# Kernel tuning notes

Hardware: AMD Instinct MI355X
Metric: run time of the kernel (lower is better)

## Reference

```python
import jax, jax.numpy as jnp
import numpy as np

DIM = 2048
N_HEADS = 32
N_KV_HEADS = 8
HEAD_DIM = 64
N_REP = N_HEADS // N_KV_HEADS
SEQ = 2048
BATCH = 1


def _llama3_scaled_rope(head_dim, end, base=10000.0, scale_factor=8):
    # matches executorch precompute_freqs_cis with use_scaled=True
    freqs = 1.0 / (base ** (np.arange(0, head_dim, 2)[: head_dim // 2] / head_dim))
    low_freq_factor, high_freq_factor, old_ctx = 1.0, 4.0, 8192.0
    low_wl = old_ctx / low_freq_factor
    high_wl = old_ctx / high_freq_factor
    wavelen = 2.0 * np.pi / freqs
    smooth = (old_ctx / wavelen - low_freq_factor) / (high_freq_factor - low_freq_factor)
    scaled = np.where(
        wavelen < high_wl,
        freqs,
        np.where(wavelen > low_wl, freqs / scale_factor,
                 (1.0 - smooth) * freqs / scale_factor + smooth * freqs),
    )
    t = np.arange(end, dtype=np.float64)
    ang = np.outer(t, scaled)
    return np.cos(ang).astype(np.float32), np.sin(ang).astype(np.float32)


def setup_inputs() -> dict:
    key = jax.random.key(0)
    kx, kq, kk, kv, ko = jax.random.split(key, 5)
    x = jax.random.normal(kx, (BATCH, SEQ, DIM), dtype=jnp.float32)
    sc = 0.02
    wq = jax.random.normal(kq, (N_HEADS * HEAD_DIM, DIM), dtype=jnp.float32) * sc
    wk = jax.random.normal(kk, (N_KV_HEADS * HEAD_DIM, DIM), dtype=jnp.float32) * sc
    wv = jax.random.normal(kv, (N_KV_HEADS * HEAD_DIM, DIM), dtype=jnp.float32) * sc
    wo = jax.random.normal(ko, (N_HEADS * HEAD_DIM, DIM), dtype=jnp.float32).T * sc
    cos, sin = _llama3_scaled_rope(HEAD_DIM, SEQ)
    return {"x": x, "freqs_cos": jnp.asarray(cos), "freqs_sin": jnp.asarray(sin),
            "wq": wq, "wk": wk, "wv": wv, "wo": wo}


def _apply_rotary(x, cos, sin):
    # x: [b, s, h, hd]; cos/sin: [s, hd//2]; interleaved-pair RoPE
    xr = x[..., 0::2]
    xi = x[..., 1::2]
    c = cos[None, :, None, :]
    s = sin[None, :, None, :]
    out_r = xr * c - xi * s
    out_i = xr * s + xi * c
    return jnp.stack([out_r, out_i], axis=-1).reshape(x.shape)


def reference(x, freqs_cos, freqs_sin, wq, wk, wv, wo):
    b, s, _ = x.shape
    q = (x @ wq.T).reshape(b, s, N_HEADS, HEAD_DIM)
    k = (x @ wk.T).reshape(b, s, N_KV_HEADS, HEAD_DIM)
    v = (x @ wv.T).reshape(b, s, N_KV_HEADS, HEAD_DIM)
    q = _apply_rotary(q, freqs_cos, freqs_sin)
    k = _apply_rotary(k, freqs_cos, freqs_sin)
    # [b, h, s, hd]
    q = q.transpose(0, 2, 1, 3)
    k = k.transpose(0, 2, 1, 3)
    v = v.transpose(0, 2, 1, 3)
    # GQA: repeat_interleave over head dim
    k = jnp.repeat(k, N_REP, axis=1)
    v = jnp.repeat(v, N_REP, axis=1)
    scale = 1.0 / jnp.sqrt(jnp.asarray(HEAD_DIM, dtype=x.dtype))
    scores = jnp.einsum("bhqd,bhkd->bhqk", q, k) * scale
    causal = jnp.tril(jnp.ones((s, s), dtype=bool))
    scores = jnp.where(causal[None, None], scores, jnp.finfo(scores.dtype).min)
    attn = jax.nn.softmax(scores, axis=-1)
    y = jnp.einsum("bhqk,bhkd->bhqd", attn, v)
    y = y.transpose(0, 2, 1, 3).reshape(b, s, N_HEADS * HEAD_DIM)
    return y @ wo.T
```

## Files before the change

kernel.cpp:

```cpp
#include <hip/hip_runtime.h>
#include <hip/hip_bf16.h>

typedef __attribute__((ext_vector_type(8))) __bf16 bf16x8;
typedef __attribute__((ext_vector_type(4))) __bf16 bf16x4;
typedef __attribute__((ext_vector_type(4))) float f32x4;

#define DIM 2048
#define SEQ 2048
#define NH 32
#define NKV 8
#define HD 64
#define QKVD 3072
#define KOFF 2048
#define VOFF 2560
#define KVDIM 512

__device__ __forceinline__ void gld16(const __bf16* g, __bf16* l) {
    __builtin_amdgcn_global_load_lds(
        (const __attribute__((address_space(1))) void*)g,
        (__attribute__((address_space(3))) void*)l, 16, 0, 0);
}

__global__ void cvt_f32_bf16(const float* __restrict__ in, __bf16* __restrict__ out, int n4) {
    int i = blockIdx.x * blockDim.x + threadIdx.x;
    if (i < n4) {
        float4 v = reinterpret_cast<const float4*>(in)[i];
        bf16x4 o;
        o[0] = (__bf16)v.x; o[1] = (__bf16)v.y; o[2] = (__bf16)v.z; o[3] = (__bf16)v.w;
        reinterpret_cast<bf16x4*>(out)[i] = o;
    }
}

__global__ __launch_bounds__(256) void transpose_v(const __bf16* __restrict__ V,
                                                   __bf16* __restrict__ VT) {
    __shared__ __bf16 t[64][72];
    const int tid = threadIdx.x;
    const int r = tid >> 2, c0 = (tid & 3) * 16;
    const int sb = blockIdx.x * 64;
    const int db = blockIdx.y * 64;
    bf16x8 a0 = *reinterpret_cast<const bf16x8*>(V + (size_t)(sb + r) * QKVD + db + c0);
    bf16x8 a1 = *reinterpret_cast<const bf16x8*>(V + (size_t)(sb + r) * QKVD + db + c0 + 8);
#pragma unroll
    for (int e = 0; e < 8; ++e) { t[c0 + e][r] = a0[e]; t[c0 + 8 + e][r] = a1[e]; }
    __syncthreads();
    bf16x8 o0 = *reinterpret_cast<const bf16x8*>(&t[r][c0]);
    bf16x8 o1 = *reinterpret_cast<const bf16x8*>(&t[r][c0 + 8]);
    *reinterpret_cast<bf16x8*>(VT + (size_t)(db + r) * SEQ + sb + c0) = o0;
    *reinterpret_cast<bf16x8*>(VT + (size_t)(db + r) * SEQ + sb + c0 + 8) = o1;
}

template <typename OutT, bool ROPE>
__global__ __launch_bounds__(256) void gemm_tn(const __bf16* __restrict__ A,
                                               const __bf16* __restrict__ B,
                                               OutT* __restrict__ C,
                                               int M, int N, int K,
                                               float scale, int scaleNlim,
                                               const float* __restrict__ fc,
                                               const float* __restrict__ fs) {
    __shared__ __align__(16) __bf16 As[2][2][128 * 32];
    __shared__ __align__(16) __bf16 Bs[2][2][64 * 32];
    const int tid = threadIdx.x;
    const int lane = tid & 63;
    const int w = tid >> 6;
    const int l15 = lane & 15, lhi = lane >> 4;
    const int mb = blockIdx.y * 128;
    const int nb = blockIdx.x * 64;
    const int wm = (w >> 1) * 64, wn = (w & 1) * 32;

    const int srow = lane >> 2, scol = (lane & 3) * 8;
    const __bf16* gA0 = A + (size_t)(mb + w * 16 + srow) * K + scol;
    const __bf16* gA1 = A + (size_t)(mb + (w + 4) * 16 + srow) * K + scol;
    const __bf16* gB0 = B + (size_t)(nb + w * 16 + srow) * K + scol;

    auto stage = [&](int kk, int buf) {
#pragma unroll
        for (int s = 0; s < 2; ++s) {
            gld16(gA0 + kk + s * 32, As[buf][s] + w * 512);
            gld16(gA1 + kk + s * 32, As[buf][s] + (w + 4) * 512);
            gld16(gB0 + kk + s * 32, Bs[buf][s] + w * 512);
        }
    };

    stage(0, 0);
    __syncthreads();

    f32x4 acc[4][2] = {};
    int cur = 0;
    for (int kk = 0; kk < K; kk += 64, cur ^= 1) {
        if (kk + 64 < K) stage(kk + 64, cur ^ 1);
#pragma unroll
        for (int s = 0; s < 2; ++s) {
            bf16x8 a[4], b[2];
#pragma unroll
            for (int i = 0; i < 4; ++i)
                a[i] = *reinterpret_cast<const bf16x8*>(&As[cur][s][(wm + i * 16 + l15) * 32 + lhi * 8]);
#pragma unroll
            for (int j = 0; j < 2; ++j)
                b[j] = *reinterpret_cast<const bf16x8*>(&Bs[cur][s][(wn + j * 16 + l15) * 32 + lhi * 8]);
#pragma unroll
            for (int i = 0; i < 4; ++i)
#pragma unroll
                for (int j = 0; j < 2; ++j)
                    acc[i][j] = __builtin_amdgcn_mfma_f32_16x16x32_bf16(a[i], b[j], acc[i][j], 0, 0, 0);
        }
        __syncthreads();
    }

    const float sc = (nb < scaleNlim) ? scale : 1.0f;
    const bool doRope = ROPE && (nb < VOFF);
#pragma unroll
    for (int i = 0; i < 4; ++i)
#pragma unroll
        for (int j = 0; j < 2; ++j)
#pragma unroll
            for (int r = 0; r < 4; ++r) {
                float v = acc[i][j][r] * sc;
                if (doRope) {
                    const int col = nb + wn + j * 16 + l15;
                    const int row = mb + wm + i * 16 + lhi * 4 + r;
                    const float vp = __shfl_xor(v, 1);
                    const int fi = (col & 63) >> 1;
                    const float cc = fc[row * 32 + fi];
                    const float ss = fs[row * 32 + fi];
                    v = (col & 1) ? (vp * ss + v * cc) : (v * cc - vp * ss);
                }
                C[(size_t)(mb + wm + i * 16 + lhi * 4 + r) * N + nb + wn + j * 16 + l15] = (OutT)v;
            }
}

__global__ __launch_bounds__(256, 4) void attn_kernel(const __bf16* __restrict__ QKV,
                                                      const __bf16* __restrict__ VT,
                                                      __bf16* __restrict__ Y) {
    const int bx = blockIdx.x;
    const int g = bx >> 8;
    const int a = (bx >> 5) & 7;
    const int h = bx & 31;
    const int qt = (g == 0) ? 31 - a : (g == 1) ? a : (g == 2) ? 23 - a : 8 + a;
    const int kvh = h >> 2;
    const int tid = threadIdx.x;
    const int lane = tid & 63;
    const int w = tid >> 6;
    const int l15 = lane & 15, lhi = lane >> 4;

    __shared__ __align__(16) __bf16 Kl[2][64 * 64];
    __shared__ __align__(16) __bf16 Vl[2][64 * 64];
    __shared__ __align__(16) __bf16 Pl[4][16 * 64];

    const __bf16* Qp = QKV + h * HD;
    const __bf16* Kp = QKV + KOFF + kvh * HD;
    const __bf16* Vth = VT + (size_t)(kvh * HD) * SEQ;

    const int sr = lane >> 3;
    const int ksc = ((lane & 7) ^ sr) * 8;
    const int rswz = (l15 & 7);

    auto stage = [&](int jt, int buf) {
        const int kvb = jt * 64;
#pragma unroll
        for (int c = 0; c < 2; ++c) {
            const int row = w * 16 + c * 8;
            gld16(Kp + (size_t)(kvb + row + sr) * QKVD + ksc, &Kl[buf][row * 64]);
            gld16(Vth + (size_t)(row + sr) * SEQ + kvb + ksc, &Vl[buf][row * 64]);
        }
    };

    const int qb = qt * 64;
    const int qrow = qb + w * 16 + l15;

    const __bf16* qptr = Qp + (size_t)qrow * QKVD;
    bf16x8 qf0 = *reinterpret_cast<const bf16x8*>(qptr + lhi * 8);
    bf16x8 qf1 = *reinterpret_cast<const bf16x8*>(qptr + 32 + lhi * 8);

    f32x4 o[4] = {};
    float mrun = -1e30f;
    float lpart = 0.f;

    const int pkey = (l15 & 7) << 1;

    stage(0, 0);
    __syncthreads();

    int cur = 0;
    for (int j = 0; j <= qt; ++j, cur ^= 1) {
        const bool pre = (j < qt);
        if (pre) stage(j + 1, cur ^ 1);

        f32x4 sacc[4];
        __builtin_amdgcn_s_setprio(1);
#pragma unroll
        for (int t = 0; t < 4; ++t) {
            const int rb = (t * 16 + l15) * 64;
            bf16x8 kf0 = *reinterpret_cast<const bf16x8*>(
                &Kl[cur][rb + ((lhi ^ rswz) * 8)]);
            bf16x8 kf1 = *reinterpret_cast<const bf16x8*>(
                &Kl[cur][rb + (((4 + lhi) ^ rswz) * 8)]);
            f32x4 z = {0.f, 0.f, 0.f, 0.f};
            z = __builtin_amdgcn_mfma_f32_16x16x32_bf16(kf0, qf0, z, 0, 0, 0);
            z = __builtin_amdgcn_mfma_f32_16x16x32_bf16(kf1, qf1, z, 0, 0, 0);
            sacc[t] = z;
        }
        __builtin_amdgcn_s_setprio(0);

        if (j == qt) {
#pragma unroll
            for (int t = 0; t < 4; ++t)
#pragma unroll
                for (int r = 0; r < 4; ++r) {
                    const int kv = j * 64 + t * 16 + lhi * 4 + r;
                    if (kv > qrow) sacc[t][r] = -1e30f;
                }
        }

        float mt[4];
#pragma unroll
        for (int t = 0; t < 4; ++t)
            mt[t] = fmaxf(fmaxf(sacc[t][0], sacc[t][1]),
                          fmaxf(sacc[t][2], sacc[t][3]));
        const float pm = fmaxf(fmaxf(mt[0], mt[1]), fmaxf(mt[2], mt[3]));

        if (!__all(pm - mrun <= 8.0f)) {
            float full = pm;
            full = fmaxf(full, __shfl_xor(full, 16));
            full = fmaxf(full, __shfl_xor(full, 32));
            const float mn = fmaxf(mrun, full);
            const float aa = exp2f(mrun - mn);
            mrun = mn;
            lpart *= aa;
            float ar[4];
#pragma unroll
            for (int r = 0; r < 4; ++r) ar[r] = __shfl(aa, lhi * 4 + r);
#pragma unroll
            for (int t = 0; t < 4; ++t)
#pragma unroll
                for (int r = 0; r < 4; ++r) o[t][r] *= ar[r];
        }

#pragma unroll
        for (int t = 0; t < 4; ++t) {
            bf16x4 pk;
#pragma unroll
            for (int r = 0; r < 4; ++r) {
                const float pv = exp2f(sacc[t][r] - mrun);
                lpart += pv;
                pk[r] = (__bf16)pv;
            }
            const int sw = (t * 4 + lhi) ^ pkey;
            *reinterpret_cast<bf16x4*>(&Pl[w][l15 * 64 + sw * 4]) = pk;
        }

        bf16x8 pf0 = *reinterpret_cast<const bf16x8*>(
            &Pl[w][l15 * 64 + (((lhi * 2) ^ pkey) * 4)]);
        bf16x8 pf1 = *reinterpret_cast<const bf16x8*>(
            &Pl[w][l15 * 64 + (((8 + lhi * 2) ^ pkey) * 4)]);
        __builtin_amdgcn_s_setprio(1);
#pragma unroll
        for (int t = 0; t < 4; ++t) {
            const int rb = (t * 16 + l15) * 64;
            bf16x8 vf0 = *reinterpret_cast<const bf16x8*>(
                &Vl[cur][rb + ((lhi ^ rswz) * 8)]);
            bf16x8 vf1 = *reinterpret_cast<const bf16x8*>(
                &Vl[cur][rb + (((4 + lhi) ^ rswz) * 8)]);
            o[t] = __builtin_amdgcn_mfma_f32_16x16x32_bf16(pf0, vf0, o[t], 0, 0, 0);
            o[t] = __builtin_amdgcn_mfma_f32_16x16x32_bf16(pf1, vf1, o[t], 0, 0, 0);
        }
        __builtin_amdgcn_s_setprio(0);

        __syncthreads();
    }

    float ls = lpart;
    ls += __shfl_xor(ls, 16);
    ls += __shfl_xor(ls, 32);
    float lr[4];
#pragma unroll
    for (int r = 0; r < 4; ++r) lr[r] = __shfl(ls, lhi * 4 + r);
#pragma unroll
    for (int t = 0; t < 4; ++t)
#pragma unroll
        for (int r = 0; r < 4; ++r) {
            const float val = o[t][r] / lr[r];
            Y[(size_t)(qb + w * 16 + lhi * 4 + r) * DIM + h * HD + t * 16 + l15] =
                (__bf16)val;
        }
}

extern "C" void kernel_launch(void* const* d_in, const int* in_sizes, int n_in,
                              void* d_out, int out_size, void* d_ws, size_t ws_size,
                              hipStream_t stream) {
    const float* x    = (const float*)d_in[0];
    const float* fcos = (const float*)d_in[1];
    const float* fsin = (const float*)d_in[2];
    const float* wq   = (const float*)d_in[3];
    const float* wk   = (const float*)d_in[4];
    const float* wv   = (const float*)d_in[5];
    const float* wo   = (const float*)d_in[6];
    float* out = (float*)d_out;

    __bf16* xb    = (__bf16*)d_ws;
    __bf16* wqkvb = xb + (size_t)SEQ * DIM;
    __bf16* wob   = wqkvb + (size_t)QKVD * DIM;
    __bf16* QKVb  = wob + (size_t)DIM * DIM;
    __bf16* Yb    = QKVb + (size_t)SEQ * QKVD;
    __bf16* VTb   = Yb + (size_t)SEQ * DIM;

    const int nx  = SEQ * DIM / 4;
    const int nw  = DIM * DIM / 4;
    const int nkv = KVDIM * DIM / 4;
    cvt_f32_bf16<<<(nx + 255) / 256, 256, 0, stream>>>(x, xb, nx);
    cvt_f32_bf16<<<(nw + 255) / 256, 256, 0, stream>>>(wq, wqkvb, nw);
    cvt_f32_bf16<<<(nkv + 255) / 256, 256, 0, stream>>>(wk, wqkvb + (size_t)KOFF * DIM, nkv);
    cvt_f32_bf16<<<(nkv + 255) / 256, 256, 0, stream>>>(wv, wqkvb + (size_t)VOFF * DIM, nkv);
    cvt_f32_bf16<<<(nw + 255) / 256, 256, 0, stream>>>(wo, wob, nw);

    gemm_tn<__bf16, true><<<dim3(QKVD / 64, SEQ / 128), 256, 0, stream>>>(
        xb, wqkvb, QKVb, SEQ, QKVD, DIM, 0.125f * 1.4426950408889634f, KOFF, fcos, fsin);

    transpose_v<<<dim3(SEQ / 64, KVDIM / 64), 256, 0, stream>>>(QKVb + VOFF, VTb);

    attn_kernel<<<dim3(1024), 256, 0, stream>>>(QKVb, VTb, Yb);

    gemm_tn<float, false><<<dim3(DIM / 64, SEQ / 128), 256, 0, stream>>>(
        Yb, wob, out, SEQ, DIM, DIM, 1.0f, 0, nullptr, nullptr);
}
```

Before: 145.8 us.

## Fuse conversions into one kernel, V transpose into QKV GEMM, shrink GEMM tiles

Replaces the five separate fp32-to-bf16 conversion launches with a single kernel that dispatches by index range. Removes the standalone V transpose kernel: the QKV GEMM epilogue now writes V columns directly in transposed layout. GEMM tiles shrink from 128x64 to 64x64 with a 4-blocks-per-CU launch bound, doubling the block count to fill more CUs. The smaller tiles lower data reuse per block and increase global traffic in exchange for occupancy and fewer launches.

```diff
diff --git a/kernel.cpp b/kernel.cpp
--- a/kernel.cpp
+++ b/kernel.cpp
@@ -21,84 +21,79 @@
         (__attribute__((address_space(3))) void*)l, 16, 0, 0);
 }
 
-__global__ void cvt_f32_bf16(const float* __restrict__ in, __bf16* __restrict__ out, int n4) {
-    int i = blockIdx.x * blockDim.x + threadIdx.x;
-    if (i < n4) {
-        float4 v = reinterpret_cast<const float4*>(in)[i];
-        bf16x4 o;
-        o[0] = (__bf16)v.x; o[1] = (__bf16)v.y; o[2] = (__bf16)v.z; o[3] = (__bf16)v.w;
-        reinterpret_cast<bf16x4*>(out)[i] = o;
-    }
-}
-
-__global__ __launch_bounds__(256) void transpose_v(const __bf16* __restrict__ V,
-                                                   __bf16* __restrict__ VT) {
-    __shared__ __bf16 t[64][72];
-    const int tid = threadIdx.x;
-    const int r = tid >> 2, c0 = (tid & 3) * 16;
-    const int sb = blockIdx.x * 64;
-    const int db = blockIdx.y * 64;
-    bf16x8 a0 = *reinterpret_cast<const bf16x8*>(V + (size_t)(sb + r) * QKVD + db + c0);
-    bf16x8 a1 = *reinterpret_cast<const bf16x8*>(V + (size_t)(sb + r) * QKVD + db + c0 + 8);
-#pragma unroll
-    for (int e = 0; e < 8; ++e) { t[c0 + e][r] = a0[e]; t[c0 + 8 + e][r] = a1[e]; }
-    __syncthreads();
-    bf16x8 o0 = *reinterpret_cast<const bf16x8*>(&t[r][c0]);
-    bf16x8 o1 = *reinterpret_cast<const bf16x8*>(&t[r][c0 + 8]);
-    *reinterpret_cast<bf16x8*>(VT + (size_t)(db + r) * SEQ + sb + c0) = o0;
-    *reinterpret_cast<bf16x8*>(VT + (size_t)(db + r) * SEQ + sb + c0 + 8) = o1;
+__global__ __launch_bounds__(256) void cvt_all(const float* __restrict__ x,
+                                               const float* __restrict__ wq,
+                                               const float* __restrict__ wk,
+                                               const float* __restrict__ wv,
+                                               const float* __restrict__ wo,
+                                               __bf16* __restrict__ xb,
+                                               __bf16* __restrict__ wqkvb,
+                                               __bf16* __restrict__ wob) {
+    const int i = blockIdx.x * blockDim.x + threadIdx.x;
+    const int NX = SEQ * DIM / 4;
+    const int NW = DIM * DIM / 4;
+    const int NKV4 = KVDIM * DIM / 4;
+    const float* src; __bf16* dst; int off;
+    if (i < NX)                        { src = x;  dst = xb;    off = i; }
+    else if (i < NX + NW)              { src = wq; dst = wqkvb; off = i - NX; }
+    else if (i < NX + NW + NKV4)       { src = wk; dst = wqkvb + (size_t)KOFF * DIM; off = i - NX - NW; }
+    else if (i < NX + NW + 2 * NKV4)   { src = wv; dst = wqkvb + (size_t)VOFF * DIM; off = i - NX - NW - NKV4; }
+    else                               { src = wo; dst = wob;   off = i - NX - NW - 2 * NKV4; }
+    float4 v = reinterpret_cast<const float4*>(src)[off];
+    bf16x4 o;
+    o[0] = (__bf16)v.x; o[1] = (__bf16)v.y; o[2] = (__bf16)v.z; o[3] = (__bf16)v.w;
+    reinterpret_cast<bf16x4*>(dst)[off] = o;
 }
 
 template <typename OutT, bool ROPE>
-__global__ __launch_bounds__(256) void gemm_tn(const __bf16* __restrict__ A,
-                                               const __bf16* __restrict__ B,
-                                               OutT* __restrict__ C,
-                                               int M, int N, int K,
-                                               float scale, int scaleNlim,
-                                               const float* __restrict__ fc,
-                                               const float* __restrict__ fs) {
-    __shared__ __align__(16) __bf16 As[2][2][128 * 32];
+__global__ __launch_bounds__(256, 4) void gemm_tn(const __bf16* __restrict__ A,
+                                                  const __bf16* __restrict__ B,
+                                                  OutT* __restrict__ C,
+                                                  int M, int N, int K,
+                                                  float scale, int scaleNlim,
+                                                  const float* __restrict__ fc,
+                                                  const float* __restrict__ fs,
+                                                  __bf16* __restrict__ VTout) {
+    __shared__ __align__(16) __bf16 As[2][2][64 * 32];
     __shared__ __align__(16) __bf16 Bs[2][2][64 * 32];
     const int tid = threadIdx.x;
     const int lane = tid & 63;
     const int w = tid >> 6;
     const int l15 = lane & 15, lhi = lane >> 4;
-    const int mb = blockIdx.y * 128;
+    const int mb = blockIdx.y * 64;
     const int nb = blockIdx.x * 64;
-    const int wm = (w >> 1) * 64, wn = (w & 1) * 32;
+    const int wm = (w >> 1) * 32, wn = (w & 1) * 32;
 
     const int srow = lane >> 2, scol = (lane & 3) * 8;
-    const __bf16* gA0 = A + (size_t)(mb + w * 16 + srow) * K + scol;
-    const __bf16* gA1 = A + (size_t)(mb + (w + 4) * 16 + srow) * K + scol;
-    const __bf16* gB0 = B + (size_t)(nb + w * 16 + srow) * K + scol;
+    const __bf16* gA = A + (size_t)(mb + w * 16 + srow) * K + scol;
+    const __bf16* gB = B + (size_t)(nb + w * 16 + srow) * K + scol;
 
     auto stage = [&](int kk, int buf) {
 #pragma unroll
         for (int s = 0; s < 2; ++s) {
-            gld16(gA0 + kk + s * 32, As[buf][s] + w * 512);
-            gld16(gA1 + kk + s * 32, As[buf][s] + (w + 4) * 512);
-            gld16(gB0 + kk + s * 32, Bs[buf][s] + w * 512);
+            gld16(gA + kk + s * 32, As[buf][s] + w * 512);
+            gld16(gB + kk + s * 32, Bs[buf][s] + w * 512);
         }
     };
 
     stage(0, 0);
     __syncthreads();
 
-    f32x4 acc[4][2] = {};
+    f32x4 acc[2][2] = {};
     int cur = 0;
     for (int kk = 0; kk < K; kk += 64, cur ^= 1) {
         if (kk + 64 < K) stage(kk + 64, cur ^ 1);
 #pragma unroll
         for (int s = 0; s < 2; ++s) {
-            bf16x8 a[4], b[2];
-#pragma unroll
-            for (int i = 0; i < 4; ++i)
+            bf16x8 a[2], b[2];
+#pragma unroll
+            for (int i = 0; i < 2; ++i)
                 a[i] = *reinterpret_cast<const bf16x8*>(&As[cur][s][(wm + i * 16 + l15) * 32 + lhi * 8]);
 #pragma unroll
             for (int j = 0; j < 2; ++j)
                 b[j] = *reinterpret_cast<const bf16x8*>(&Bs[cur][s][(wn + j * 16 + l15) * 32 + lhi * 8]);
 #pragma unroll
-            for (int i = 0; i < 4; ++i)
+            for (int i = 0; i < 2; ++i)
 #pragma unroll
                 for (int j = 0; j < 2; ++j)
                     acc[i][j] = __builtin_amdgcn_mfma_f32_16x16x32_bf16(a[i], b[j], acc[i][j], 0, 0, 0);
@@ -106,26 +101,41 @@
         __syncthreads();
     }
 
-    const float sc = (nb < scaleNlim) ? scale : 1.0f;
-    const bool doRope = ROPE && (nb < VOFF);
-#pragma unroll
-    for (int i = 0; i < 4; ++i)
-#pragma unroll
-        for (int j = 0; j < 2; ++j)
-#pragma unroll
-            for (int r = 0; r < 4; ++r) {
-                float v = acc[i][j][r] * sc;
-                if (doRope) {
-                    const int col = nb + wn + j * 16 + l15;
-                    const int row = mb + wm + i * 16 + lhi * 4 + r;
-                    const float vp = __shfl_xor(v, 1);
-                    const int fi = (col & 63) >> 1;
-                    const float cc = fc[row * 32 + fi];
-                    const float ss = fs[row * 32 + fi];
-                    v = (col & 1) ? (vp * ss + v * cc) : (v * cc - vp * ss);
+    const bool toVT = ROPE && (VTout != nullptr) && (nb >= VOFF);
+    if (toVT) {
+#pragma unroll
+        for (int i = 0; i < 2; ++i)
+#pragma unroll
+            for (int j = 0; j < 2; ++j) {
+                bf16x4 pv;
+#pragma unroll
+                for (int r = 0; r < 4; ++r) pv[r] = (__bf16)acc[i][j][r];
+                const int colv = nb - VOFF + wn + j * 16 + l15;
+                const int row0 = mb + wm + i * 16 + lhi * 4;
+                *reinterpret_cast<bf16x4*>(VTout + (size_t)colv * M + row0) = pv;
+            }
+    } else {
+        const float sc = (nb < scaleNlim) ? scale : 1.0f;
+        const bool doRope = ROPE && (nb < VOFF);
+#pragma unroll
+        for (int i = 0; i < 2; ++i)
+#pragma unroll
+            for (int j = 0; j < 2; ++j)
+#pragma unroll
+                for (int r = 0; r < 4; ++r) {
+                    float v = acc[i][j][r] * sc;
+                    if (doRope) {
+                        const int col = nb + wn + j * 16 + l15;
+                        const int row = mb + wm + i * 16 + lhi * 4 + r;
+                        const float vp = __shfl_xor(v, 1);
+                        const int fi = (col & 63) >> 1;
+                        const float cc = fc[row * 32 + fi];
+                        const float ss = fs[row * 32 + fi];
+                        v = (col & 1) ? (vp * ss + v * cc) : (v * cc - vp * ss);
+                    }
+                    C[(size_t)(mb + wm + i * 16 + lhi * 4 + r) * N + nb + wn + j * 16 + l15] = (OutT)v;
                 }
-                C[(size_t)(mb + wm + i * 16 + lhi * 4 + r) * N + nb + wn + j * 16 + l15] = (OutT)v;
-            }
+    }
 }
 
 __global__ __launch_bounds__(256, 4) void attn_kernel(const __bf16* __restrict__ QKV,
@@ -303,22 +313,15 @@
     __bf16* Yb    = QKVb + (size_t)SEQ * QKVD;
     __bf16* VTb   = Yb + (size_t)SEQ * DIM;
 
-    const int nx  = SEQ * DIM / 4;
-    const int nw  = DIM * DIM / 4;
-    const int nkv = KVDIM * DIM / 4;
-    cvt_f32_bf16<<<(nx + 255) / 256, 256, 0, stream>>>(x, xb, nx);
-    cvt_f32_bf16<<<(nw + 255) / 256, 256, 0, stream>>>(wq, wqkvb, nw);
-    cvt_f32_bf16<<<(nkv + 255) / 256, 256, 0, stream>>>(wk, wqkvb + (size_t)KOFF * DIM, nkv);
-    cvt_f32_bf16<<<(nkv + 255) / 256, 256, 0, stream>>>(wv, wqkvb + (size_t)VOFF * DIM, nkv);
-    cvt_f32_bf16<<<(nw + 255) / 256, 256, 0, stream>>>(wo, wob, nw);
-
-    gemm_tn<__bf16, true><<<dim3(QKVD / 64, SEQ / 128), 256, 0, stream>>>(
-        xb, wqkvb, QKVb, SEQ, QKVD, DIM, 0.125f * 1.4426950408889634f, KOFF, fcos, fsin);
-
-    transpose_v<<<dim3(SEQ / 64, KVDIM / 64), 256, 0, stream>>>(QKVb + VOFF, VTb);
+    const int ncvt = (SEQ * DIM / 4) + 2 * (DIM * DIM / 4) + 2 * (KVDIM * DIM / 4);
+    cvt_all<<<ncvt / 256, 256, 0, stream>>>(x, wq, wk, wv, wo, xb, wqkvb, wob);
+
+    gemm_tn<__bf16, true><<<dim3(QKVD / 64, SEQ / 64), 256, 0, stream>>>(
+        xb, wqkvb, QKVb, SEQ, QKVD, DIM, 0.125f * 1.4426950408889634f, KOFF,
+        fcos, fsin, VTb);
 
     attn_kernel<<<dim3(1024), 256, 0, stream>>>(QKVb, VTb, Yb);
 
-    gemm_tn<float, false><<<dim3(DIM / 64, SEQ / 128), 256, 0, stream>>>(
-        Yb, wob, out, SEQ, DIM, DIM, 1.0f, 0, nullptr, nullptr);
-}
+    gemm_tn<float, false><<<dim3(DIM / 64, SEQ / 64), 256, 0, stream>>>(
+        Yb, wob, out, SEQ, DIM, DIM, 1.0f, 0, nullptr, nullptr, nullptr);
+}
```

Measured after the change: 150.1 us. 1.03x slower.
